# Performance work log

Hardware: AMD Instinct MI355X
Metric: run time of the kernel (lower is better)

## Reference

```python
import jax, jax.numpy as jnp
import numpy as np
from jax import lax

SAMPLE_RATE = 0.25
RADIUS = 0.5
NSAMPLE = 32
MLP = [64 + 3, 64, 128]  # use_xyz adds 3 to first width


def setup_inputs() -> dict:
    key = jax.random.key(0)
    ks = jax.random.split(key, 8)
    B, N, C = 8, 8192, 64
    pos = jax.random.normal(ks[0], (B, N, 3), dtype=jnp.float32)
    features = jax.random.normal(ks[1], (B, C, N), dtype=jnp.float32)
    # shared MLP (1x1 Conv2d with bias, ReLU), He-scaled init
    w0 = jax.random.normal(ks[2], (MLP[1], MLP[0]), jnp.float32) * (2.0 / MLP[0]) ** 0.5
    b0 = jnp.zeros((MLP[1],), jnp.float32)
    w1 = jax.random.normal(ks[3], (MLP[1], MLP[1]), jnp.float32) * (2.0 / MLP[1]) ** 0.5
    b1 = jnp.zeros((MLP[1],), jnp.float32)
    w2 = jax.random.normal(ks[4], (MLP[2], MLP[1]), jnp.float32) * (2.0 / MLP[1]) ** 0.5
    b2 = jnp.zeros((MLP[2],), jnp.float32)
    return {"pos": pos, "features": features, "w0": w0, "b0": b0,
            "w1": w1, "b1": b1, "w2": w2, "b2": b2}


def furthest_point_sample(pos, npoint):
    """pos: (B,N,3) -> idx (B,npoint) int32, greedy FPS starting at index 0."""
    B, N, _ = pos.shape
    init_idx = jnp.zeros((B,), jnp.int32)
    init_d = jnp.full((B, N), 1e10, jnp.float32)

    def step(carry, _):
        dists, last = carry
        p_last = jnp.take_along_axis(pos, last[:, None, None], axis=1)  # (B,1,3)
        d = jnp.sum((pos - p_last) ** 2, axis=-1)                        # (B,N)
        dists = jnp.minimum(dists, d)
        nxt = jnp.argmax(dists, axis=-1).astype(jnp.int32)
        return (dists, nxt), nxt

    (_, _), rest = lax.scan(step, (init_d, init_idx), None, length=npoint - 1)
    return jnp.concatenate([init_idx[None, :], rest], axis=0).T  # (B,npoint)


def ball_query(pos, new_xyz, nsample, radius):
    """pos (B,N,3), new_xyz (B,S,3) -> idx (B,S,nsample): first nsample pts
    within radius, padded with the first hit (0 if no hit), as in PointNet2 CUDA."""
    B, N, _ = pos.shape
    d2 = jnp.sum((new_xyz[:, :, None, :] - pos[:, None, :, :]) ** 2, axis=-1)  # (B,S,N)
    cand = jnp.where(d2 < radius * radius,
                     jnp.arange(N, dtype=jnp.int32)[None, None, :], N)
    neg_top, _ = lax.top_k(-cand, nsample)     # smallest nsample indices
    idx = -neg_top                              # ascending index order
    first = idx[..., :1]
    pad = jnp.where(first == N, 0, first)
    return jnp.where(idx == N, pad, idx)


def reference(pos, features, w0, b0, w1, b1, w2, b2):
    B, N, _ = pos.shape
    npoint = int(N * SAMPLE_RATE)
    fps_idx = furthest_point_sample(pos, npoint)                         # (B,S)
    new_xyz = jax.vmap(lambda p, i: p[i])(pos, fps_idx)                  # (B,S,3)

    idx = ball_query(pos, new_xyz, NSAMPLE, RADIUS)                      # (B,S,K)
    grouped_xyz = jax.vmap(lambda p, i: p[i])(pos, idx)                  # (B,S,K,3)
    rel_xyz = grouped_xyz - new_xyz[:, :, None, :]                       # (B,S,K,3)
    grouped_feat = jax.vmap(lambda f, i: f[:, i])(features, idx)         # (B,C,S,K)
    x = jnp.concatenate([rel_xyz.transpose(0, 3, 1, 2), grouped_feat], axis=1)  # (B,3+C,S,K)

    def conv_relu(x, w, b):  # 1x1 conv + bias + ReLU
        y = jnp.einsum('oc,bcsk->bosk', w, x) + b[None, :, None, None]
        return jax.nn.relu(y)

    x = conv_relu(x, w0, b0)
    x = conv_relu(x, w1, b1)
    x = conv_relu(x, w2, b2)
    new_features = jnp.max(x, axis=-1)                                   # (B,mlp[-1],S)
    return new_xyz, new_features
```

## Files before the change

kernel.cpp:

```cpp
#include <hip/hip_runtime.h>

#define NB 8
#define NPTS 8192
#define NC_FEAT 64
#define NS 2048
#define NK 32

typedef float v2f __attribute__((ext_vector_type(2)));

__device__ __forceinline__ float d2_ref(float px, float py, float pz,
                                        float qx, float qy, float qz) {
  float dx = __fsub_rn(px, qx);
  float dy = __fsub_rn(py, qy);
  float dz = __fsub_rn(pz, qz);
  return __fadd_rn(__fadd_rn(__fmul_rn(dx, dx), __fmul_rn(dy, dy)),
                   __fmul_rn(dz, dz));
}

#define DPP_KEYMAX(key, ctrl)                                                 \
  {                                                                           \
    unsigned _lo = (unsigned)__builtin_amdgcn_update_dpp(                     \
        0, (int)(unsigned)(key), (ctrl), 0xf, 0xf, true);                     \
    unsigned _hi = (unsigned)__builtin_amdgcn_update_dpp(                     \
        0, (int)(unsigned)((key) >> 32), (ctrl), 0xf, 0xf, true);             \
    unsigned long long _o = ((unsigned long long)_hi << 32) | _lo;            \
    if (_o > (key)) (key) = _o;                                               \
  }

__global__ __launch_bounds__(512)
void k_fps(const float* __restrict__ pos, float* __restrict__ new_xyz) {
#pragma clang fp contract(off)
  __shared__ __align__(16) float smem[3 * NPTS + 64];
  const int tid = threadIdx.x;
  const int b = blockIdx.x;
  float* sx = smem;
  float* sy = smem + NPTS;
  float* sz = smem + 2 * NPTS;
  unsigned long long* rk = (unsigned long long*)(smem + 3 * NPTS);

  const float* p = pos + (size_t)b * NPTS * 3;
  for (int i = tid; i < NPTS; i += 512) {
    sx[i] = p[3 * i + 0];
    sy[i] = p[3 * i + 1];
    sz[i] = p[3 * i + 2];
  }
  if (tid < 32) rk[tid] = 0ull;
  __syncthreads();

  const int base = tid * 16;
  v2f px[8], py[8], pz[8], di[8];
#pragma unroll
  for (int k = 0; k < 8; ++k) {
    px[k] = (v2f){sx[base + 2 * k], sx[base + 2 * k + 1]};
    py[k] = (v2f){sy[base + 2 * k], sy[base + 2 * k + 1]};
    pz[k] = (v2f){sz[base + 2 * k], sz[base + 2 * k + 1]};
    di[k] = (v2f){1e10f, 1e10f};
  }
  if (tid == 0) {
    new_xyz[((size_t)b * NS) * 3 + 0] = sx[0];
    new_xyz[((size_t)b * NS) * 3 + 1] = sy[0];
    new_xyz[((size_t)b * NS) * 3 + 2] = sz[0];
  }

  const int lane = tid & 63;
  const int wave = tid >> 6;
  const unsigned nbase = ~(unsigned)base;
  int last = 0, buf = 0;

  for (int it = 1; it < NS; ++it) {
    float qx = sx[last], qy = sy[last], qz = sz[last];
#pragma unroll
    for (int k = 0; k < 8; ++k) {
      v2f dx = px[k] - qx;
      v2f dy = py[k] - qy;
      v2f dz = pz[k] - qz;
      v2f d2 = (dx * dx + dy * dy) + dz * dz;
      di[k] = __builtin_elementwise_min(di[k], d2);
    }
    v2f m0 = __builtin_elementwise_max(di[0], di[1]);
    v2f m1 = __builtin_elementwise_max(di[2], di[3]);
    v2f m2 = __builtin_elementwise_max(di[4], di[5]);
    v2f m3 = __builtin_elementwise_max(di[6], di[7]);
    v2f m4 = __builtin_elementwise_max(m0, m1);
    v2f m5 = __builtin_elementwise_max(m2, m3);
    v2f m6 = __builtin_elementwise_max(m4, m5);
    float bd = fmaxf(m6.x, m6.y);
    int bj = 0;
#pragma unroll
    for (int j = 15; j >= 0; --j) {
      float v = (j & 1) ? di[j >> 1].y : di[j >> 1].x;
      if (v == bd) bj = j;
    }
    unsigned long long key =
        ((unsigned long long)__float_as_uint(bd) << 32) |
        (unsigned)(nbase - (unsigned)bj);
    DPP_KEYMAX(key, 0x111);
    DPP_KEYMAX(key, 0x112);
    DPP_KEYMAX(key, 0x114);
    DPP_KEYMAX(key, 0x118);
    DPP_KEYMAX(key, 0x142);
    DPP_KEYMAX(key, 0x143);
    if (lane == 63) rk[buf * 16 + wave] = key;
    __syncthreads();
    key = rk[buf * 16 + (lane & 15)];
    DPP_KEYMAX(key, 0x111);
    DPP_KEYMAX(key, 0x112);
    DPP_KEYMAX(key, 0x114);
    DPP_KEYMAX(key, 0x118);
    int fi = (int)~(unsigned)__builtin_amdgcn_readlane((int)(unsigned)key, 15);
    last = fi;
    buf ^= 1;
    if (tid == 0) {
      new_xyz[((size_t)b * NS + it) * 3 + 0] = sx[fi];
      new_xyz[((size_t)b * NS + it) * 3 + 1] = sy[fi];
      new_xyz[((size_t)b * NS + it) * 3 + 2] = sz[fi];
    }
  }
}

__global__ __launch_bounds__(256)
void k_tp(const float* __restrict__ feat, const float* __restrict__ w0,
          const float* __restrict__ w1, const float* __restrict__ w2,
          float* __restrict__ featT, float* __restrict__ wT) {
  __shared__ float tile[64 * 65];
  const int tid = threadIdx.x;
  if (blockIdx.x < NB * (NPTS / 64)) {
    const int t = blockIdx.x;
    const int b = t >> 7;
    const int n0 = (t & 127) << 6;
    const int col = tid & 63;
    const int r0 = tid >> 6;
#pragma unroll
    for (int q = 0; q < 16; ++q) {
      int c = r0 + q * 4;
      tile[c * 65 + col] = feat[((size_t)b * NC_FEAT + c) * NPTS + n0 + col];
    }
    __syncthreads();
#pragma unroll
    for (int q = 0; q < 16; ++q) {
      int r = r0 + q * 4;
      featT[((size_t)b * NPTS + n0 + r) * 64 + col] = tile[col * 65 + r];
    }
  } else {
    for (int i = tid; i < 67 * 64; i += 256)
      wT[i] = w0[(i & 63) * 67 + (i >> 6)];
    for (int i = tid; i < 64 * 64; i += 256)
      wT[67 * 64 + i] = w1[(i & 63) * 64 + (i >> 6)];
    for (int i = tid; i < 64 * 128; i += 256)
      wT[67 * 64 + 64 * 64 + i] = w2[(i & 127) * 64 + (i >> 7)];
  }
}

__global__ __launch_bounds__(256)
void k_ball(const float* __restrict__ pos, const float* __restrict__ nxyz,
            int* __restrict__ ballidx) {
  const int wid = (blockIdx.x * 256 + threadIdx.x) >> 6;
  const int lane = threadIdx.x & 63;
  const int b = wid >> 11;
  const float qx = nxyz[wid * 3 + 0];
  const float qy = nxyz[wid * 3 + 1];
  const float qz = nxyz[wid * 3 + 2];
  const float* p = pos + (size_t)b * NPTS * 3;
  int* outp = ballidx + (size_t)wid * NK;

  int cnt = 0;
  int firstidx = 0x7fffffff;
  for (int n0 = 0; n0 < NPTS; n0 += 64) {
    const int i = n0 + lane;
    float d2 = d2_ref(p[3 * i], p[3 * i + 1], p[3 * i + 2], qx, qy, qz);
    bool hit = d2 < 0.25f;
    unsigned long long mask = __ballot(hit);
    int pre = __popcll(mask & ((1ull << lane) - 1ull));
    int slot = cnt + pre;
    if (hit && slot < NK) outp[slot] = i;
    if (hit && slot == 0) firstidx = i;
    cnt += __popcll(mask);
    if (cnt >= NK) break;
  }
#pragma unroll
  for (int m = 32; m >= 1; m >>= 1)
    firstidx = min(firstidx, __shfl_xor(firstidx, m, 64));
  int pad = (firstidx == 0x7fffffff) ? 0 : firstidx;
  int start = cnt < NK ? cnt : NK;
  if (lane < NK && lane >= start) outp[lane] = pad;
}

#define MLP_FMA16(wr, xc, acc)                                   \
  _Pragma("unroll") for (int o4 = 0; o4 < 16; ++o4) {            \
    float4 w = (wr)[o4];                                         \
    (acc)[o4 * 4 + 0] = fmaf(w.x, (xc), (acc)[o4 * 4 + 0]);      \
    (acc)[o4 * 4 + 1] = fmaf(w.y, (xc), (acc)[o4 * 4 + 1]);      \
    (acc)[o4 * 4 + 2] = fmaf(w.z, (xc), (acc)[o4 * 4 + 2]);      \
    (acc)[o4 * 4 + 3] = fmaf(w.w, (xc), (acc)[o4 * 4 + 3]);      \
  }

__global__ __launch_bounds__(256)
void k_mlp(const float* __restrict__ pos, const float* __restrict__ featT,
           const float* __restrict__ wT, const float* __restrict__ b0,
           const float* __restrict__ b1, const float* __restrict__ b2,
           const int* __restrict__ ballidx, const float* __restrict__ nxyz,
           float* __restrict__ outf) {
  __shared__ float xs[64 * 256];
  const int tid = threadIdx.x;
  const int g = blockIdx.x * 256 + tid;
  const int s = (g >> 5) & (NS - 1);
  const int b = g >> 16;

  const int idx = ballidx[g];
  const float qx = nxyz[((size_t)b * NS + s) * 3 + 0];
  const float qy = nxyz[((size_t)b * NS + s) * 3 + 1];
  const float qz = nxyz[((size_t)b * NS + s) * 3 + 2];
  const float* pp = pos + ((size_t)b * NPTS + idx) * 3;
  const float x0 = __fsub_rn(pp[0], qx);
  const float x1 = __fsub_rn(pp[1], qy);
  const float x2 = __fsub_rn(pp[2], qz);

  const float4* fT = (const float4*)(featT + ((size_t)b * NPTS + idx) * 64);
#pragma unroll
  for (int c4 = 0; c4 < 16; ++c4) {
    float4 v = fT[c4];
    xs[(c4 * 4 + 0) * 256 + tid] = v.x;
    xs[(c4 * 4 + 1) * 256 + tid] = v.y;
    xs[(c4 * 4 + 2) * 256 + tid] = v.z;
    xs[(c4 * 4 + 3) * 256 + tid] = v.w;
  }

  const float* wt0 = wT;
  const float* wt1 = wT + 67 * 64;
  const float* wt2 = wT + 67 * 64 + 64 * 64;

  float acc[64];
#pragma unroll
  for (int o = 0; o < 64; ++o) acc[o] = b0[o];
  {
    const float xr0 = x0, xr1 = x1, xr2 = x2;
    const float4* wr;
    wr = (const float4*)(wt0 + 0 * 64); MLP_FMA16(wr, xr0, acc);
    wr = (const float4*)(wt0 + 1 * 64); MLP_FMA16(wr, xr1, acc);
    wr = (const float4*)(wt0 + 2 * 64); MLP_FMA16(wr, xr2, acc);
  }
  for (int c = 0; c < 64; ++c) {
    float xc = xs[c * 256 + tid];
    const float4* wr = (const float4*)(wt0 + (3 + c) * 64);
    MLP_FMA16(wr, xc, acc);
  }
#pragma unroll
  for (int o = 0; o < 64; ++o) xs[o * 256 + tid] = fmaxf(acc[o], 0.0f);

#pragma unroll
  for (int o = 0; o < 64; ++o) acc[o] = b1[o];
  for (int c = 0; c < 64; ++c) {
    float xc = xs[c * 256 + tid];
    const float4* wr = (const float4*)(wt1 + c * 64);
    MLP_FMA16(wr, xc, acc);
  }
#pragma unroll
  for (int o = 0; o < 64; ++o) xs[o * 256 + tid] = fmaxf(acc[o], 0.0f);

#pragma unroll
  for (int h = 0; h < 2; ++h) {
#pragma unroll
    for (int o = 0; o < 64; ++o) acc[o] = b2[h * 64 + o];
    for (int c = 0; c < 64; ++c) {
      float xc = xs[c * 256 + tid];
      const float4* wr = (const float4*)(wt2 + c * 128 + h * 64);
      MLP_FMA16(wr, xc, acc);
    }
#pragma unroll
    for (int o = 0; o < 64; ++o) {
      float v = fmaxf(acc[o], 0.0f);
      v = fmaxf(v, __shfl_xor(v, 16, 64));
      v = fmaxf(v, __shfl_xor(v, 8, 64));
      v = fmaxf(v, __shfl_xor(v, 4, 64));
      v = fmaxf(v, __shfl_xor(v, 2, 64));
      v = fmaxf(v, __shfl_xor(v, 1, 64));
      if ((tid & 31) == 0)
        outf[((size_t)b * 128 + h * 64 + o) * NS + s] = v;
    }
  }
}

extern "C" void kernel_launch(void* const* d_in, const int* in_sizes, int n_in,
                              void* d_out, int out_size, void* d_ws,
                              size_t ws_size, hipStream_t stream) {
  const float* pos = (const float*)d_in[0];
  const float* feat = (const float*)d_in[1];
  const float* w0 = (const float*)d_in[2];
  const float* b0 = (const float*)d_in[3];
  const float* w1 = (const float*)d_in[4];
  const float* b1 = (const float*)d_in[5];
  const float* w2 = (const float*)d_in[6];
  const float* b2 = (const float*)d_in[7];

  float* out = (float*)d_out;
  float* new_xyz = out;
  float* new_feat = out + (size_t)NB * NS * 3;

  int* ballidx = (int*)d_ws;
  float* featT = (float*)d_ws + (size_t)NB * NS * NK;
  float* wT = featT + (size_t)NB * NPTS * 64;

  hipLaunchKernelGGL(k_tp, dim3(NB * (NPTS / 64) + 1), dim3(256), 0, stream,
                     feat, w0, w1, w2, featT, wT);
  hipLaunchKernelGGL(k_fps, dim3(NB), dim3(512), 0, stream, pos, new_xyz);
  hipLaunchKernelGGL(k_ball, dim3((NB * NS) / 4), dim3(256), 0, stream, pos,
                     new_xyz, ballidx);
  hipLaunchKernelGGL(k_mlp, dim3((NB * NS * NK) / 256), dim3(256), 0, stream,
                     pos, featT, wT, b0, b1, b2, ballidx, new_xyz, new_feat);
}
```

Measured before the change: 2.457 ms.

## Morton-sort points in FPS and skip distance updates for far thread clusters

The FPS kernel now computes a bounding box, quantizes points to 10-bit Morton codes and bitonic-sorts them in shared memory so each thread owns a spatially compact cluster. Each thread keeps a bounding sphere and skips its distance-update and local argmax when the newly selected point is too far away to lower any of its distances, reusing its cached key. Tie-breaking keys now encode the original index so results match the reference's lowest-index argmax. This adds a one-off sort with many barriers and more shared memory, and the skip check depends on the float margins being conservative.

```diff
diff --git a/kernel.cpp b/kernel.cpp
--- a/kernel.cpp
+++ b/kernel.cpp
@@ -27,93 +27,224 @@
     if (_o > (key)) (key) = _o;                                               \
   }
 
+#define DPP_FMIN(v, ctrl)                                                     \
+  {                                                                           \
+    float _o = __int_as_float(__builtin_amdgcn_update_dpp(                    \
+        __float_as_int(v), __float_as_int(v), (ctrl), 0xf, 0xf, false));      \
+    (v) = fminf((v), _o);                                                     \
+  }
+#define DPP_FMAX(v, ctrl)                                                     \
+  {                                                                           \
+    float _o = __int_as_float(__builtin_amdgcn_update_dpp(                    \
+        __float_as_int(v), __float_as_int(v), (ctrl), 0xf, 0xf, false));      \
+    (v) = fmaxf((v), _o);                                                     \
+  }
+#define DPP_RED6_FMIN(v) \
+  DPP_FMIN(v, 0x111); DPP_FMIN(v, 0x112); DPP_FMIN(v, 0x114); \
+  DPP_FMIN(v, 0x118); DPP_FMIN(v, 0x142); DPP_FMIN(v, 0x143)
+#define DPP_RED6_FMAX(v) \
+  DPP_FMAX(v, 0x111); DPP_FMAX(v, 0x112); DPP_FMAX(v, 0x114); \
+  DPP_FMAX(v, 0x118); DPP_FMAX(v, 0x142); DPP_FMAX(v, 0x143)
+
+__device__ __forceinline__ unsigned msp(unsigned x) {
+  x &= 0x3FF;
+  x = (x | (x << 16)) & 0x030000FF;
+  x = (x | (x << 8)) & 0x0300F00F;
+  x = (x | (x << 4)) & 0x030C30C3;
+  x = (x | (x << 2)) & 0x09249249;
+  return x;
+}
+
 __global__ __launch_bounds__(512)
 void k_fps(const float* __restrict__ pos, float* __restrict__ new_xyz) {
 #pragma clang fp contract(off)
-  __shared__ __align__(16) float smem[3 * NPTS + 64];
-  const int tid = threadIdx.x;
-  const int b = blockIdx.x;
+  __shared__ __align__(16) float smem[4 * NPTS + 128];
   float* sx = smem;
   float* sy = smem + NPTS;
   float* sz = smem + 2 * NPTS;
-  unsigned long long* rk = (unsigned long long*)(smem + 3 * NPTS);
-
+  unsigned* K = (unsigned*)smem;
+  unsigned* P = (unsigned*)(smem + 3 * NPTS);
+  unsigned long long* rk = (unsigned long long*)(smem + 4 * NPTS);
+  float* wavebb = smem + 4 * NPTS + 64;
+  float* bbx = smem + 4 * NPTS + 64 + 48;
+  int* last0p = (int*)(smem + 4 * NPTS + 64 + 48 + 6);
+
+  const int tid = threadIdx.x;
+  const int b = blockIdx.x;
+  const int lane = tid & 63;
+  const int wave = tid >> 6;
   const float* p = pos + (size_t)b * NPTS * 3;
+
+  float mnx = 3e38f, mny = 3e38f, mnz = 3e38f;
+  float mxx = -3e38f, mxy = -3e38f, mxz = -3e38f;
   for (int i = tid; i < NPTS; i += 512) {
-    sx[i] = p[3 * i + 0];
-    sy[i] = p[3 * i + 1];
-    sz[i] = p[3 * i + 2];
+    float x = p[3 * i], y = p[3 * i + 1], z = p[3 * i + 2];
+    mnx = fminf(mnx, x); mxx = fmaxf(mxx, x);
+    mny = fminf(mny, y); mxy = fmaxf(mxy, y);
+    mnz = fminf(mnz, z); mxz = fmaxf(mxz, z);
+  }
+  DPP_RED6_FMIN(mnx); DPP_RED6_FMIN(mny); DPP_RED6_FMIN(mnz);
+  DPP_RED6_FMAX(mxx); DPP_RED6_FMAX(mxy); DPP_RED6_FMAX(mxz);
+  if (lane == 63) {
+    wavebb[wave * 6 + 0] = mnx; wavebb[wave * 6 + 1] = mny;
+    wavebb[wave * 6 + 2] = mnz; wavebb[wave * 6 + 3] = mxx;
+    wavebb[wave * 6 + 4] = mxy; wavebb[wave * 6 + 5] = mxz;
+  }
+  __syncthreads();
+  if (tid == 0) {
+    float a0 = 3e38f, a1 = 3e38f, a2 = 3e38f;
+    float a3 = -3e38f, a4 = -3e38f, a5 = -3e38f;
+    for (int w = 0; w < 8; ++w) {
+      a0 = fminf(a0, wavebb[w * 6 + 0]); a1 = fminf(a1, wavebb[w * 6 + 1]);
+      a2 = fminf(a2, wavebb[w * 6 + 2]); a3 = fmaxf(a3, wavebb[w * 6 + 3]);
+      a4 = fmaxf(a4, wavebb[w * 6 + 4]); a5 = fmaxf(a5, wavebb[w * 6 + 5]);
+    }
+    bbx[0] = a0; bbx[1] = a1; bbx[2] = a2;
+    bbx[3] = 1023.0f / fmaxf(a3 - a0, 1e-30f);
+    bbx[4] = 1023.0f / fmaxf(a4 - a1, 1e-30f);
+    bbx[5] = 1023.0f / fmaxf(a5 - a2, 1e-30f);
+  }
+  __syncthreads();
+  const float ox = bbx[0], oy = bbx[1], oz = bbx[2];
+  const float gx = bbx[3], gy = bbx[4], gz = bbx[5];
+
+  for (int i = tid; i < NPTS; i += 512) {
+    float x = p[3 * i], y = p[3 * i + 1], z = p[3 * i + 2];
+    unsigned ux = (unsigned)fminf(fmaxf((x - ox) * gx, 0.0f), 1023.0f);
+    unsigned uy = (unsigned)fminf(fmaxf((y - oy) * gy, 0.0f), 1023.0f);
+    unsigned uz = (unsigned)fminf(fmaxf((z - oz) * gz, 0.0f), 1023.0f);
+    K[i] = msp(ux) | (msp(uy) << 1) | (msp(uz) << 2);
+    P[i] = (unsigned)i;
+  }
+
+  for (int k2 = 2; k2 <= NPTS; k2 <<= 1) {
+    for (int j = k2 >> 1; j > 0; j >>= 1) {
+      __syncthreads();
+      for (int t = 0; t < 16; ++t) {
+        int i = t * 512 + tid;
+        int ixj = i ^ j;
+        if (ixj > i) {
+          unsigned a = K[i], c = K[ixj];
+          bool up = ((i & k2) == 0);
+          if ((a > c) == up) {
+            K[i] = c; K[ixj] = a;
+            unsigned pa = P[i]; P[i] = P[ixj]; P[ixj] = pa;
+          }
+        }
+      }
+    }
+  }
+  __syncthreads();
+
+  for (int i = tid; i < NPTS; i += 512) {
+    unsigned u = P[i];
+    if (u == 0) *last0p = i;
+    sx[i] = p[3 * u];
+    sy[i] = p[3 * u + 1];
+    sz[i] = p[3 * u + 2];
   }
   if (tid < 32) rk[tid] = 0ull;
   __syncthreads();
 
   const int base = tid * 16;
   v2f px[8], py[8], pz[8], di[8];
+  unsigned opk[8];
 #pragma unroll
   for (int k = 0; k < 8; ++k) {
     px[k] = (v2f){sx[base + 2 * k], sx[base + 2 * k + 1]};
     py[k] = (v2f){sy[base + 2 * k], sy[base + 2 * k + 1]};
     pz[k] = (v2f){sz[base + 2 * k], sz[base + 2 * k + 1]};
     di[k] = (v2f){1e10f, 1e10f};
-  }
+    opk[k] = (P[base + 2 * k] & 0xFFFF) | (P[base + 2 * k + 1] << 16);
+  }
+  float lmnx = 3e38f, lmny = 3e38f, lmnz = 3e38f;
+  float lmxx = -3e38f, lmxy = -3e38f, lmxz = -3e38f;
+#pragma unroll
+  for (int k = 0; k < 8; ++k) {
+    lmnx = fminf(lmnx, fminf(px[k].x, px[k].y));
+    lmxx = fmaxf(lmxx, fmaxf(px[k].x, px[k].y));
+    lmny = fminf(lmny, fminf(py[k].x, py[k].y));
+    lmxy = fmaxf(lmxy, fmaxf(py[k].x, py[k].y));
+    lmnz = fminf(lmnz, fminf(pz[k].x, pz[k].y));
+    lmxz = fmaxf(lmxz, fmaxf(pz[k].x, pz[k].y));
+  }
+  const float cx = (lmnx + lmxx) * 0.5f;
+  const float cy = (lmny + lmxy) * 0.5f;
+  const float cz = (lmnz + lmxz) * 0.5f;
+  float r2m = 0.0f;
+#pragma unroll
+  for (int k = 0; k < 8; ++k) {
+    r2m = fmaxf(r2m, d2_ref(px[k].x, py[k].x, pz[k].x, cx, cy, cz));
+    r2m = fmaxf(r2m, d2_ref(px[k].y, py[k].y, pz[k].y, cx, cy, cz));
+  }
+  const float r = sqrtf(r2m) * 1.001f;
+  float T = 3.4e38f;
+  unsigned long long key = 0;
+
+  int last = *last0p;
   if (tid == 0) {
-    new_xyz[((size_t)b * NS) * 3 + 0] = sx[0];
-    new_xyz[((size_t)b * NS) * 3 + 1] = sy[0];
-    new_xyz[((size_t)b * NS) * 3 + 2] = sz[0];
-  }
-
-  const int lane = tid & 63;
-  const int wave = tid >> 6;
-  const unsigned nbase = ~(unsigned)base;
-  int last = 0, buf = 0;
+    new_xyz[((size_t)b * NS) * 3 + 0] = sx[last];
+    new_xyz[((size_t)b * NS) * 3 + 1] = sy[last];
+    new_xyz[((size_t)b * NS) * 3 + 2] = sz[last];
+  }
+  int buf = 0;
 
   for (int it = 1; it < NS; ++it) {
     float qx = sx[last], qy = sy[last], qz = sz[last];
-#pragma unroll
-    for (int k = 0; k < 8; ++k) {
-      v2f dx = px[k] - qx;
-      v2f dy = py[k] - qy;
-      v2f dz = pz[k] - qz;
-      v2f d2 = (dx * dx + dy * dy) + dz * dz;
-      di[k] = __builtin_elementwise_min(di[k], d2);
-    }
-    v2f m0 = __builtin_elementwise_max(di[0], di[1]);
-    v2f m1 = __builtin_elementwise_max(di[2], di[3]);
-    v2f m2 = __builtin_elementwise_max(di[4], di[5]);
-    v2f m3 = __builtin_elementwise_max(di[6], di[7]);
-    v2f m4 = __builtin_elementwise_max(m0, m1);
-    v2f m5 = __builtin_elementwise_max(m2, m3);
-    v2f m6 = __builtin_elementwise_max(m4, m5);
-    float bd = fmaxf(m6.x, m6.y);
-    int bj = 0;
-#pragma unroll
-    for (int j = 15; j >= 0; --j) {
-      float v = (j & 1) ? di[j >> 1].y : di[j >> 1].x;
-      if (v == bd) bj = j;
-    }
-    unsigned long long key =
-        ((unsigned long long)__float_as_uint(bd) << 32) |
-        (unsigned)(nbase - (unsigned)bj);
-    DPP_KEYMAX(key, 0x111);
-    DPP_KEYMAX(key, 0x112);
-    DPP_KEYMAX(key, 0x114);
-    DPP_KEYMAX(key, 0x118);
-    DPP_KEYMAX(key, 0x142);
-    DPP_KEYMAX(key, 0x143);
-    if (lane == 63) rk[buf * 16 + wave] = key;
+    float ddx = cx - qx, ddy = cy - qy, ddz = cz - qz;
+    float dc2 = ddx * ddx + ddy * ddy + ddz * ddz;
+    if (dc2 <= T) {
+#pragma unroll
+      for (int k = 0; k < 8; ++k) {
+        v2f dx = px[k] - qx;
+        v2f dy = py[k] - qy;
+        v2f dz = pz[k] - qz;
+        v2f d2 = (dx * dx + dy * dy) + dz * dz;
+        di[k] = __builtin_elementwise_min(di[k], d2);
+      }
+      v2f m0 = __builtin_elementwise_max(di[0], di[1]);
+      v2f m1 = __builtin_elementwise_max(di[2], di[3]);
+      v2f m2 = __builtin_elementwise_max(di[4], di[5]);
+      v2f m3 = __builtin_elementwise_max(di[6], di[7]);
+      v2f m4 = __builtin_elementwise_max(m0, m1);
+      v2f m5 = __builtin_elementwise_max(m2, m3);
+      v2f m6 = __builtin_elementwise_max(m4, m5);
+      float bd = fmaxf(m6.x, m6.y);
+      int bj = 0;
+      unsigned oj = 0;
+#pragma unroll
+      for (int j = 15; j >= 0; --j) {
+        float v = (j & 1) ? di[j >> 1].y : di[j >> 1].x;
+        unsigned o = (j & 1) ? (opk[j >> 1] >> 16) : (opk[j >> 1] & 0xFFFF);
+        if (v == bd) { bj = j; oj = o; }
+      }
+      key = ((unsigned long long)__float_as_uint(bd) << 32) |
+            ((unsigned long long)((~oj) & 0x1FFFu) << 13) |
+            (unsigned)(base + bj);
+      float t1 = sqrtf(bd) * 1.001f + r;
+      T = t1 * t1 * 1.002f;
+    }
+    unsigned long long wk = key;
+    DPP_KEYMAX(wk, 0x111);
+    DPP_KEYMAX(wk, 0x112);
+    DPP_KEYMAX(wk, 0x114);
+    DPP_KEYMAX(wk, 0x118);
+    DPP_KEYMAX(wk, 0x142);
+    DPP_KEYMAX(wk, 0x143);
+    if (lane == 63) rk[buf * 16 + wave] = wk;
     __syncthreads();
-    key = rk[buf * 16 + (lane & 15)];
-    DPP_KEYMAX(key, 0x111);
-    DPP_KEYMAX(key, 0x112);
-    DPP_KEYMAX(key, 0x114);
-    DPP_KEYMAX(key, 0x118);
-    int fi = (int)~(unsigned)__builtin_amdgcn_readlane((int)(unsigned)key, 15);
-    last = fi;
+    wk = rk[buf * 16 + (lane & 15)];
+    DPP_KEYMAX(wk, 0x111);
+    DPP_KEYMAX(wk, 0x112);
+    DPP_KEYMAX(wk, 0x114);
+    DPP_KEYMAX(wk, 0x118);
+    last = (int)((unsigned)__builtin_amdgcn_readlane((int)(unsigned)wk, 15) &
+                 0x1FFFu);
     buf ^= 1;
     if (tid == 0) {
-      new_xyz[((size_t)b * NS + it) * 3 + 0] = sx[fi];
-      new_xyz[((size_t)b * NS + it) * 3 + 1] = sy[fi];
-      new_xyz[((size_t)b * NS + it) * 3 + 2] = sz[fi];
+      new_xyz[((size_t)b * NS + it) * 3 + 0] = sx[last];
+      new_xyz[((size_t)b * NS + it) * 3 + 1] = sy[last];
+      new_xyz[((size_t)b * NS + it) * 3 + 2] = sz[last];
     }
   }
 }
```

Result: slower. 3.304 ms (+34.5%).

## Shrink FPS block to 256 threads with 32 points per thread and inline-asm distance

Applied to the files above, without the earlier changes.

The furthest-point-sampling kernel now runs 4 waves of 256 threads, each holding 32 points in registers instead of 16. Fewer waves shorten the cross-wave reduction: only 4 partial keys go through shared memory, and the second DPP stage drops to two steps. The distance update is written as packed-f32 inline assembly, and a running argmax is kept inside the loop instead of a separate max tree plus equality scan. The trade is double the serial per-thread work on each iteration in exchange for cheaper synchronisation; the FPS launch is only 8 blocks, so latency is set by the per-block critical path.

```diff
diff --git a/kernel.cpp b/kernel.cpp
--- a/kernel.cpp
+++ b/kernel.cpp
@@ -27,33 +27,34 @@
     if (_o > (key)) (key) = _o;                                               \
   }
 
-__global__ __launch_bounds__(512)
+__global__ __launch_bounds__(256)
 void k_fps(const float* __restrict__ pos, float* __restrict__ new_xyz) {
 #pragma clang fp contract(off)
-  __shared__ __align__(16) float smem[3 * NPTS + 64];
-  const int tid = threadIdx.x;
-  const int b = blockIdx.x;
+  __shared__ __align__(16) float smem[3 * NPTS + 16];
   float* sx = smem;
   float* sy = smem + NPTS;
   float* sz = smem + 2 * NPTS;
   unsigned long long* rk = (unsigned long long*)(smem + 3 * NPTS);
 
+  const int tid = threadIdx.x;
+  const int b = blockIdx.x;
   const float* p = pos + (size_t)b * NPTS * 3;
-  for (int i = tid; i < NPTS; i += 512) {
+
+  for (int i = tid; i < NPTS; i += 256) {
     sx[i] = p[3 * i + 0];
     sy[i] = p[3 * i + 1];
     sz[i] = p[3 * i + 2];
   }
-  if (tid < 32) rk[tid] = 0ull;
+  if (tid < 8) rk[tid] = 0ull;
   __syncthreads();
 
-  const int base = tid * 16;
-  v2f px[8], py[8], pz[8], di[8];
-#pragma unroll
-  for (int k = 0; k < 8; ++k) {
-    px[k] = (v2f){sx[base + 2 * k], sx[base + 2 * k + 1]};
-    py[k] = (v2f){sy[base + 2 * k], sy[base + 2 * k + 1]};
-    pz[k] = (v2f){sz[base + 2 * k], sz[base + 2 * k + 1]};
+  const int base = tid * 32;
+  v2f px[16], py[16], pz[16], di[16];
+#pragma unroll
+  for (int k = 0; k < 16; ++k) {
+    px[k] = *(const v2f*)&sx[base + 2 * k];
+    py[k] = *(const v2f*)&sy[base + 2 * k];
+    pz[k] = *(const v2f*)&sz[base + 2 * k];
     di[k] = (v2f){1e10f, 1e10f};
   }
   if (tid == 0) {
@@ -64,50 +65,47 @@
 
   const int lane = tid & 63;
   const int wave = tid >> 6;
-  const unsigned nbase = ~(unsigned)base;
   int last = 0, buf = 0;
 
   for (int it = 1; it < NS; ++it) {
     float qx = sx[last], qy = sy[last], qz = sz[last];
-#pragma unroll
-    for (int k = 0; k < 8; ++k) {
-      v2f dx = px[k] - qx;
-      v2f dy = py[k] - qy;
-      v2f dz = pz[k] - qz;
-      v2f d2 = (dx * dx + dy * dy) + dz * dz;
-      di[k] = __builtin_elementwise_min(di[k], d2);
-    }
-    v2f m0 = __builtin_elementwise_max(di[0], di[1]);
-    v2f m1 = __builtin_elementwise_max(di[2], di[3]);
-    v2f m2 = __builtin_elementwise_max(di[4], di[5]);
-    v2f m3 = __builtin_elementwise_max(di[6], di[7]);
-    v2f m4 = __builtin_elementwise_max(m0, m1);
-    v2f m5 = __builtin_elementwise_max(m2, m3);
-    v2f m6 = __builtin_elementwise_max(m4, m5);
-    float bd = fmaxf(m6.x, m6.y);
+    v2f nqx = (v2f){-qx, -qx};
+    v2f nqy = (v2f){-qy, -qy};
+    v2f nqz = (v2f){-qz, -qz};
+    float bd = -1.0f;
     int bj = 0;
 #pragma unroll
-    for (int j = 15; j >= 0; --j) {
-      float v = (j & 1) ? di[j >> 1].y : di[j >> 1].x;
-      if (v == bd) bj = j;
+    for (int k = 0; k < 16; ++k) {
+      v2f t0, t1, t2, d2v;
+      asm("v_pk_add_f32 %0, %4, %7\n\t"
+          "v_pk_add_f32 %1, %5, %8\n\t"
+          "v_pk_add_f32 %2, %6, %9\n\t"
+          "v_pk_mul_f32 %0, %0, %0\n\t"
+          "v_pk_mul_f32 %1, %1, %1\n\t"
+          "v_pk_mul_f32 %2, %2, %2\n\t"
+          "v_pk_add_f32 %3, %0, %1\n\t"
+          "v_pk_add_f32 %3, %3, %2"
+          : "=&v"(t0), "=&v"(t1), "=&v"(t2), "=&v"(d2v)
+          : "v"(px[k]), "v"(py[k]), "v"(pz[k]), "v"(nqx), "v"(nqy), "v"(nqz));
+      di[k] = __builtin_elementwise_min(di[k], d2v);
+      if (di[k].x > bd) { bd = di[k].x; bj = 2 * k; }
+      if (di[k].y > bd) { bd = di[k].y; bj = 2 * k + 1; }
     }
     unsigned long long key =
         ((unsigned long long)__float_as_uint(bd) << 32) |
-        (unsigned)(nbase - (unsigned)bj);
+        (unsigned)~(unsigned)(base + bj);
     DPP_KEYMAX(key, 0x111);
     DPP_KEYMAX(key, 0x112);
     DPP_KEYMAX(key, 0x114);
     DPP_KEYMAX(key, 0x118);
     DPP_KEYMAX(key, 0x142);
     DPP_KEYMAX(key, 0x143);
-    if (lane == 63) rk[buf * 16 + wave] = key;
+    if (lane == 63) rk[buf * 4 + wave] = key;
     __syncthreads();
-    key = rk[buf * 16 + (lane & 15)];
+    key = rk[buf * 4 + (lane & 3)];
     DPP_KEYMAX(key, 0x111);
     DPP_KEYMAX(key, 0x112);
-    DPP_KEYMAX(key, 0x114);
-    DPP_KEYMAX(key, 0x118);
-    int fi = (int)~(unsigned)__builtin_amdgcn_readlane((int)(unsigned)key, 15);
+    int fi = (int)~(unsigned)__builtin_amdgcn_readlane((int)(unsigned)key, 3);
     last = fi;
     buf ^= 1;
     if (tid == 0) {
@@ -302,7 +300,7 @@
 
   hipLaunchKernelGGL(k_tp, dim3(NB * (NPTS / 64) + 1), dim3(256), 0, stream,
                      feat, w0, w1, w2, featT, wT);
-  hipLaunchKernelGGL(k_fps, dim3(NB), dim3(512), 0, stream, pos, new_xyz);
+  hipLaunchKernelGGL(k_fps, dim3(NB), dim3(256), 0, stream, pos, new_xyz);
   hipLaunchKernelGGL(k_ball, dim3((NB * NS) / 4), dim3(256), 0, stream, pos,
                      new_xyz, ballidx);
   hipLaunchKernelGGL(k_mlp, dim3((NB * NS * NK) / 256), dim3(256), 0, stream,
```

Result: slower. 2.524 ms (+2.7%).

## Fuse FPS, ball query and MLP into one persistent kernel with progress flags

Applied to the files above, without the earlier changes.

Replaces the separate FPS, ball-query and MLP launches with one persistent kernel. The first 8 blocks run FPS and publish sampled centroids plus a progress counter through global atomics. The remaining blocks pull 16-centroid tasks from an atomic queue, spin until FPS has reached those centroids, then run ball query into shared memory and the MLP. This overlaps the serial FPS phase with downstream work and removes the ball-index round trip through global memory, but it depends on co-residency of the FPS blocks with the spinning workers and adds polling overhead.

```diff
diff --git a/kernel.cpp b/kernel.cpp
--- a/kernel.cpp
+++ b/kernel.cpp
@@ -5,8 +5,16 @@
 #define NC_FEAT 64
 #define NS 2048
 #define NK 32
+#define NTASK (NB * NS)
 
 typedef float v2f __attribute__((ext_vector_type(2)));
+
+#define WS_QUEUE 0
+#define WS_PROG 64
+#define WS_XY64 4096
+#define WS_Z32 (4096 + 131072)
+#define WS_FEATT (4096 + 131072 + 65536)
+#define WS_WT (WS_FEATT + (size_t)NB * NPTS * 64 * 4)
 
 __device__ __forceinline__ float d2_ref(float px, float py, float pz,
                                         float qx, float qy, float qz) {
@@ -27,102 +35,22 @@
     if (_o > (key)) (key) = _o;                                               \
   }
 
-__global__ __launch_bounds__(512)
-void k_fps(const float* __restrict__ pos, float* __restrict__ new_xyz) {
-#pragma clang fp contract(off)
-  __shared__ __align__(16) float smem[3 * NPTS + 64];
-  const int tid = threadIdx.x;
-  const int b = blockIdx.x;
-  float* sx = smem;
-  float* sy = smem + NPTS;
-  float* sz = smem + 2 * NPTS;
-  unsigned long long* rk = (unsigned long long*)(smem + 3 * NPTS);
-
-  const float* p = pos + (size_t)b * NPTS * 3;
-  for (int i = tid; i < NPTS; i += 512) {
-    sx[i] = p[3 * i + 0];
-    sy[i] = p[3 * i + 1];
-    sz[i] = p[3 * i + 2];
-  }
-  if (tid < 32) rk[tid] = 0ull;
-  __syncthreads();
-
-  const int base = tid * 16;
-  v2f px[8], py[8], pz[8], di[8];
-#pragma unroll
-  for (int k = 0; k < 8; ++k) {
-    px[k] = (v2f){sx[base + 2 * k], sx[base + 2 * k + 1]};
-    py[k] = (v2f){sy[base + 2 * k], sy[base + 2 * k + 1]};
-    pz[k] = (v2f){sz[base + 2 * k], sz[base + 2 * k + 1]};
-    di[k] = (v2f){1e10f, 1e10f};
-  }
-  if (tid == 0) {
-    new_xyz[((size_t)b * NS) * 3 + 0] = sx[0];
-    new_xyz[((size_t)b * NS) * 3 + 1] = sy[0];
-    new_xyz[((size_t)b * NS) * 3 + 2] = sz[0];
-  }
-
-  const int lane = tid & 63;
-  const int wave = tid >> 6;
-  const unsigned nbase = ~(unsigned)base;
-  int last = 0, buf = 0;
-
-  for (int it = 1; it < NS; ++it) {
-    float qx = sx[last], qy = sy[last], qz = sz[last];
-#pragma unroll
-    for (int k = 0; k < 8; ++k) {
-      v2f dx = px[k] - qx;
-      v2f dy = py[k] - qy;
-      v2f dz = pz[k] - qz;
-      v2f d2 = (dx * dx + dy * dy) + dz * dz;
-      di[k] = __builtin_elementwise_min(di[k], d2);
-    }
-    v2f m0 = __builtin_elementwise_max(di[0], di[1]);
-    v2f m1 = __builtin_elementwise_max(di[2], di[3]);
-    v2f m2 = __builtin_elementwise_max(di[4], di[5]);
-    v2f m3 = __builtin_elementwise_max(di[6], di[7]);
-    v2f m4 = __builtin_elementwise_max(m0, m1);
-    v2f m5 = __builtin_elementwise_max(m2, m3);
-    v2f m6 = __builtin_elementwise_max(m4, m5);
-    float bd = fmaxf(m6.x, m6.y);
-    int bj = 0;
-#pragma unroll
-    for (int j = 15; j >= 0; --j) {
-      float v = (j & 1) ? di[j >> 1].y : di[j >> 1].x;
-      if (v == bd) bj = j;
-    }
-    unsigned long long key =
-        ((unsigned long long)__float_as_uint(bd) << 32) |
-        (unsigned)(nbase - (unsigned)bj);
-    DPP_KEYMAX(key, 0x111);
-    DPP_KEYMAX(key, 0x112);
-    DPP_KEYMAX(key, 0x114);
-    DPP_KEYMAX(key, 0x118);
-    DPP_KEYMAX(key, 0x142);
-    DPP_KEYMAX(key, 0x143);
-    if (lane == 63) rk[buf * 16 + wave] = key;
-    __syncthreads();
-    key = rk[buf * 16 + (lane & 15)];
-    DPP_KEYMAX(key, 0x111);
-    DPP_KEYMAX(key, 0x112);
-    DPP_KEYMAX(key, 0x114);
-    DPP_KEYMAX(key, 0x118);
-    int fi = (int)~(unsigned)__builtin_amdgcn_readlane((int)(unsigned)key, 15);
-    last = fi;
-    buf ^= 1;
-    if (tid == 0) {
-      new_xyz[((size_t)b * NS + it) * 3 + 0] = sx[fi];
-      new_xyz[((size_t)b * NS + it) * 3 + 1] = sy[fi];
-      new_xyz[((size_t)b * NS + it) * 3 + 2] = sz[fi];
-    }
-  }
-}
+#define MLP_FMA16(wr, xc, acc)                                   \
+  _Pragma("unroll") for (int o4 = 0; o4 < 16; ++o4) {            \
+    float4 w = (wr)[o4];                                         \
+    (acc)[o4 * 4 + 0] = fmaf(w.x, (xc), (acc)[o4 * 4 + 0]);      \
+    (acc)[o4 * 4 + 1] = fmaf(w.y, (xc), (acc)[o4 * 4 + 1]);      \
+    (acc)[o4 * 4 + 2] = fmaf(w.z, (xc), (acc)[o4 * 4 + 2]);      \
+    (acc)[o4 * 4 + 3] = fmaf(w.w, (xc), (acc)[o4 * 4 + 3]);      \
+  }
 
 __global__ __launch_bounds__(256)
 void k_tp(const float* __restrict__ feat, const float* __restrict__ w0,
           const float* __restrict__ w1, const float* __restrict__ w2,
-          float* __restrict__ featT, float* __restrict__ wT) {
+          char* __restrict__ ws) {
   __shared__ float tile[64 * 65];
+  float* featT = (float*)(ws + WS_FEATT);
+  float* wT = (float*)(ws + WS_WT);
   const int tid = threadIdx.x;
   if (blockIdx.x < NB * (NPTS / 64)) {
     const int t = blockIdx.x;
@@ -142,6 +70,7 @@
       featT[((size_t)b * NPTS + n0 + r) * 64 + col] = tile[col * 65 + r];
     }
   } else {
+    if (tid < 24) ((int*)ws)[tid] = 0;
     for (int i = tid; i < 67 * 64; i += 256)
       wT[i] = w0[(i & 63) * 67 + (i >> 6)];
     for (int i = tid; i < 64 * 64; i += 256)
@@ -151,132 +80,268 @@
   }
 }
 
-__global__ __launch_bounds__(256)
-void k_ball(const float* __restrict__ pos, const float* __restrict__ nxyz,
-            int* __restrict__ ballidx) {
-  const int wid = (blockIdx.x * 256 + threadIdx.x) >> 6;
-  const int lane = threadIdx.x & 63;
-  const int b = wid >> 11;
-  const float qx = nxyz[wid * 3 + 0];
-  const float qy = nxyz[wid * 3 + 1];
-  const float qz = nxyz[wid * 3 + 2];
-  const float* p = pos + (size_t)b * NPTS * 3;
-  int* outp = ballidx + (size_t)wid * NK;
-
-  int cnt = 0;
-  int firstidx = 0x7fffffff;
-  for (int n0 = 0; n0 < NPTS; n0 += 64) {
-    const int i = n0 + lane;
-    float d2 = d2_ref(p[3 * i], p[3 * i + 1], p[3 * i + 2], qx, qy, qz);
-    bool hit = d2 < 0.25f;
-    unsigned long long mask = __ballot(hit);
-    int pre = __popcll(mask & ((1ull << lane) - 1ull));
-    int slot = cnt + pre;
-    if (hit && slot < NK) outp[slot] = i;
-    if (hit && slot == 0) firstidx = i;
-    cnt += __popcll(mask);
-    if (cnt >= NK) break;
-  }
-#pragma unroll
-  for (int m = 32; m >= 1; m >>= 1)
-    firstidx = min(firstidx, __shfl_xor(firstidx, m, 64));
-  int pad = (firstidx == 0x7fffffff) ? 0 : firstidx;
-  int start = cnt < NK ? cnt : NK;
-  if (lane < NK && lane >= start) outp[lane] = pad;
-}
-
-#define MLP_FMA16(wr, xc, acc)                                   \
-  _Pragma("unroll") for (int o4 = 0; o4 < 16; ++o4) {            \
-    float4 w = (wr)[o4];                                         \
-    (acc)[o4 * 4 + 0] = fmaf(w.x, (xc), (acc)[o4 * 4 + 0]);      \
-    (acc)[o4 * 4 + 1] = fmaf(w.y, (xc), (acc)[o4 * 4 + 1]);      \
-    (acc)[o4 * 4 + 2] = fmaf(w.z, (xc), (acc)[o4 * 4 + 2]);      \
-    (acc)[o4 * 4 + 3] = fmaf(w.w, (xc), (acc)[o4 * 4 + 3]);      \
-  }
-
-__global__ __launch_bounds__(256)
-void k_mlp(const float* __restrict__ pos, const float* __restrict__ featT,
-           const float* __restrict__ wT, const float* __restrict__ b0,
-           const float* __restrict__ b1, const float* __restrict__ b2,
-           const int* __restrict__ ballidx, const float* __restrict__ nxyz,
-           float* __restrict__ outf) {
-  __shared__ float xs[64 * 256];
-  const int tid = threadIdx.x;
-  const int g = blockIdx.x * 256 + tid;
-  const int s = (g >> 5) & (NS - 1);
-  const int b = g >> 16;
-
-  const int idx = ballidx[g];
-  const float qx = nxyz[((size_t)b * NS + s) * 3 + 0];
-  const float qy = nxyz[((size_t)b * NS + s) * 3 + 1];
-  const float qz = nxyz[((size_t)b * NS + s) * 3 + 2];
-  const float* pp = pos + ((size_t)b * NPTS + idx) * 3;
-  const float x0 = __fsub_rn(pp[0], qx);
-  const float x1 = __fsub_rn(pp[1], qy);
-  const float x2 = __fsub_rn(pp[2], qz);
-
-  const float4* fT = (const float4*)(featT + ((size_t)b * NPTS + idx) * 64);
-#pragma unroll
-  for (int c4 = 0; c4 < 16; ++c4) {
-    float4 v = fT[c4];
-    xs[(c4 * 4 + 0) * 256 + tid] = v.x;
-    xs[(c4 * 4 + 1) * 256 + tid] = v.y;
-    xs[(c4 * 4 + 2) * 256 + tid] = v.z;
-    xs[(c4 * 4 + 3) * 256 + tid] = v.w;
-  }
-
-  const float* wt0 = wT;
-  const float* wt1 = wT + 67 * 64;
-  const float* wt2 = wT + 67 * 64 + 64 * 64;
-
-  float acc[64];
-#pragma unroll
-  for (int o = 0; o < 64; ++o) acc[o] = b0[o];
-  {
-    const float xr0 = x0, xr1 = x1, xr2 = x2;
-    const float4* wr;
-    wr = (const float4*)(wt0 + 0 * 64); MLP_FMA16(wr, xr0, acc);
-    wr = (const float4*)(wt0 + 1 * 64); MLP_FMA16(wr, xr1, acc);
-    wr = (const float4*)(wt0 + 2 * 64); MLP_FMA16(wr, xr2, acc);
-  }
-  for (int c = 0; c < 64; ++c) {
-    float xc = xs[c * 256 + tid];
-    const float4* wr = (const float4*)(wt0 + (3 + c) * 64);
-    MLP_FMA16(wr, xc, acc);
-  }
-#pragma unroll
-  for (int o = 0; o < 64; ++o) xs[o * 256 + tid] = fmaxf(acc[o], 0.0f);
-
-#pragma unroll
-  for (int o = 0; o < 64; ++o) acc[o] = b1[o];
-  for (int c = 0; c < 64; ++c) {
-    float xc = xs[c * 256 + tid];
-    const float4* wr = (const float4*)(wt1 + c * 64);
-    MLP_FMA16(wr, xc, acc);
-  }
-#pragma unroll
-  for (int o = 0; o < 64; ++o) xs[o * 256 + tid] = fmaxf(acc[o], 0.0f);
-
-#pragma unroll
-  for (int h = 0; h < 2; ++h) {
-#pragma unroll
-    for (int o = 0; o < 64; ++o) acc[o] = b2[h * 64 + o];
-    for (int c = 0; c < 64; ++c) {
-      float xc = xs[c * 256 + tid];
-      const float4* wr = (const float4*)(wt2 + c * 128 + h * 64);
-      MLP_FMA16(wr, xc, acc);
-    }
-#pragma unroll
-    for (int o = 0; o < 64; ++o) {
-      float v = fmaxf(acc[o], 0.0f);
-      v = fmaxf(v, __shfl_xor(v, 16, 64));
-      v = fmaxf(v, __shfl_xor(v, 8, 64));
-      v = fmaxf(v, __shfl_xor(v, 4, 64));
-      v = fmaxf(v, __shfl_xor(v, 2, 64));
-      v = fmaxf(v, __shfl_xor(v, 1, 64));
-      if ((tid & 31) == 0)
-        outf[((size_t)b * 128 + h * 64 + o) * NS + s] = v;
-    }
+__global__ __launch_bounds__(512)
+void k_fused(const float* __restrict__ pos, const float* __restrict__ b0,
+             const float* __restrict__ b1, const float* __restrict__ b2,
+             char* __restrict__ ws, float* __restrict__ new_xyz,
+             float* __restrict__ outf) {
+#pragma clang fp contract(off)
+  __shared__ __align__(16) float smf[33360];
+  int* queue = (int*)ws;
+  int* progress = (int*)(ws + WS_PROG);
+  unsigned long long* xy64 = (unsigned long long*)(ws + WS_XY64);
+  unsigned* z32 = (unsigned*)(ws + WS_Z32);
+  const float* featT = (const float*)(ws + WS_FEATT);
+  const float* wT = (const float*)(ws + WS_WT);
+  const int wtid = threadIdx.x;
+
+  if (blockIdx.x < NB) {
+    float* sx = smf;
+    float* sy = smf + NPTS;
+    float* sz = smf + 2 * NPTS;
+    unsigned long long* rk = (unsigned long long*)(smf + 3 * NPTS);
+    const int tid = wtid;
+    const int b = blockIdx.x;
+    const float* p = pos + (size_t)b * NPTS * 3;
+
+    for (int i = tid; i < NPTS; i += 512) {
+      sx[i] = p[3 * i + 0];
+      sy[i] = p[3 * i + 1];
+      sz[i] = p[3 * i + 2];
+    }
+    if (tid < 32) rk[tid] = 0ull;
+    __syncthreads();
+
+    const int base = tid * 16;
+    v2f px[8], py[8], pz[8], di[8];
+#pragma unroll
+    for (int k = 0; k < 8; ++k) {
+      px[k] = *(const v2f*)&sx[base + 2 * k];
+      py[k] = *(const v2f*)&sy[base + 2 * k];
+      pz[k] = *(const v2f*)&sz[base + 2 * k];
+      di[k] = (v2f){1e10f, 1e10f};
+    }
+    if (tid == 0) {
+      new_xyz[((size_t)b * NS) * 3 + 0] = sx[0];
+      new_xyz[((size_t)b * NS) * 3 + 1] = sy[0];
+      new_xyz[((size_t)b * NS) * 3 + 2] = sz[0];
+      unsigned long long xy = ((unsigned long long)__float_as_uint(sy[0]) << 32) |
+                              __float_as_uint(sx[0]);
+      __hip_atomic_store(&xy64[b * NS + 0], xy, __ATOMIC_RELAXED,
+                         __HIP_MEMORY_SCOPE_AGENT);
+      __hip_atomic_store(&z32[b * NS + 0], __float_as_uint(sz[0]),
+                         __ATOMIC_RELAXED, __HIP_MEMORY_SCOPE_AGENT);
+    }
+
+    const int lane = tid & 63;
+    const int wave = tid >> 6;
+    int last = 0, buf = 0;
+
+    for (int it = 1; it < NS; ++it) {
+      float qx = sx[last], qy = sy[last], qz = sz[last];
+#pragma unroll
+      for (int k = 0; k < 8; ++k) {
+        v2f dx = px[k] - qx;
+        v2f dy = py[k] - qy;
+        v2f dz = pz[k] - qz;
+        v2f d2 = (dx * dx + dy * dy) + dz * dz;
+        di[k] = __builtin_elementwise_min(di[k], d2);
+      }
+      v2f m0 = __builtin_elementwise_max(di[0], di[1]);
+      v2f m1 = __builtin_elementwise_max(di[2], di[3]);
+      v2f m2 = __builtin_elementwise_max(di[4], di[5]);
+      v2f m3 = __builtin_elementwise_max(di[6], di[7]);
+      v2f m4 = __builtin_elementwise_max(m0, m1);
+      v2f m5 = __builtin_elementwise_max(m2, m3);
+      v2f m6 = __builtin_elementwise_max(m4, m5);
+      float bd = fmaxf(m6.x, m6.y);
+      int bj = 0;
+#pragma unroll
+      for (int j = 15; j >= 0; --j) {
+        float v = (j & 1) ? di[j >> 1].y : di[j >> 1].x;
+        if (v == bd) bj = j;
+      }
+      unsigned long long key =
+          ((unsigned long long)__float_as_uint(bd) << 32) |
+          (unsigned)~(unsigned)(base + bj);
+      DPP_KEYMAX(key, 0x111);
+      DPP_KEYMAX(key, 0x112);
+      DPP_KEYMAX(key, 0x114);
+      DPP_KEYMAX(key, 0x118);
+      DPP_KEYMAX(key, 0x142);
+      DPP_KEYMAX(key, 0x143);
+      if (lane == 63) rk[buf * 16 + wave] = key;
+      __syncthreads();
+      key = rk[buf * 16 + (lane & 15)];
+      DPP_KEYMAX(key, 0x111);
+      DPP_KEYMAX(key, 0x112);
+      DPP_KEYMAX(key, 0x114);
+      DPP_KEYMAX(key, 0x118);
+      int fi = (int)~(unsigned)__builtin_amdgcn_readlane((int)(unsigned)key, 15);
+      last = fi;
+      buf ^= 1;
+      if (tid == 0) {
+        float fx = sx[fi], fy = sy[fi], fz = sz[fi];
+        new_xyz[((size_t)b * NS + it) * 3 + 0] = fx;
+        new_xyz[((size_t)b * NS + it) * 3 + 1] = fy;
+        new_xyz[((size_t)b * NS + it) * 3 + 2] = fz;
+        unsigned long long xy =
+            ((unsigned long long)__float_as_uint(fy) << 32) | __float_as_uint(fx);
+        __hip_atomic_store(&xy64[b * NS + it], xy, __ATOMIC_RELAXED,
+                           __HIP_MEMORY_SCOPE_AGENT);
+        __hip_atomic_store(&z32[b * NS + it], __float_as_uint(fz),
+                           __ATOMIC_RELAXED, __HIP_MEMORY_SCOPE_AGENT);
+        if ((it & 31) == 31)
+          __hip_atomic_store(&progress[b], it + 1, __ATOMIC_RELEASE,
+                             __HIP_MEMORY_SCOPE_AGENT);
+      }
+    }
+    return;
+  }
+
+  float* xs0 = smf;
+  int* sidx = (int*)(smf + 32768);
+  float* snx = smf + 32768 + 512;
+  int* sbase = (int*)(smf + 32768 + 512 + 64);
+  const int lane = wtid & 63;
+  const int w = wtid >> 6;
+
+  for (;;) {
+    if (wtid == 0) *sbase = atomicAdd(queue, 16);
+    __syncthreads();
+    const int base_t = *sbase;
+    if (base_t >= NTASK) break;
+    const int sEnd = ((base_t + 15) >> 3) + 1;
+    if (wtid < 64) {
+      int pr;
+      do {
+        __builtin_amdgcn_s_sleep(2);
+        pr = (lane < 8) ? __hip_atomic_load(&progress[lane], __ATOMIC_ACQUIRE,
+                                            __HIP_MEMORY_SCOPE_AGENT)
+                        : 0x7fffffff;
+      } while (!__all(pr >= sEnd));
+    }
+    __syncthreads();
+    if (wtid < 16) {
+      int t = base_t + wtid, bb = t & 7, ss = t >> 3;
+      unsigned long long xy = __hip_atomic_load(
+          &xy64[bb * NS + ss], __ATOMIC_RELAXED, __HIP_MEMORY_SCOPE_AGENT);
+      unsigned z = __hip_atomic_load(&z32[bb * NS + ss], __ATOMIC_RELAXED,
+                                     __HIP_MEMORY_SCOPE_AGENT);
+      snx[wtid * 4 + 0] = __uint_as_float((unsigned)xy);
+      snx[wtid * 4 + 1] = __uint_as_float((unsigned)(xy >> 32));
+      snx[wtid * 4 + 2] = __uint_as_float(z);
+    }
+    __syncthreads();
+#pragma unroll
+    for (int tt = 0; tt < 2; ++tt) {
+      const int tl = w * 2 + tt;
+      const int bb = (base_t + tl) & 7;
+      const float qx = snx[tl * 4 + 0];
+      const float qy = snx[tl * 4 + 1];
+      const float qz = snx[tl * 4 + 2];
+      const float* p = pos + (size_t)bb * NPTS * 3;
+      int cnt = 0;
+      int firstidx = 0x7fffffff;
+      for (int n0 = 0; n0 < NPTS; n0 += 64) {
+        const int i = n0 + lane;
+        float d2 = d2_ref(p[3 * i], p[3 * i + 1], p[3 * i + 2], qx, qy, qz);
+        bool hit = d2 < 0.25f;
+        unsigned long long mask = __ballot(hit);
+        int pre = __popcll(mask & ((1ull << lane) - 1ull));
+        int slot = cnt + pre;
+        if (hit && slot < NK) sidx[tl * 32 + slot] = i;
+        if (hit && slot == 0) firstidx = i;
+        cnt += __popcll(mask);
+        if (cnt >= NK) break;
+      }
+#pragma unroll
+      for (int m = 32; m >= 1; m >>= 1)
+        firstidx = min(firstidx, __shfl_xor(firstidx, m, 64));
+      int pad = (firstidx == 0x7fffffff) ? 0 : firstidx;
+      int start = cnt < NK ? cnt : NK;
+      if (lane < NK && lane >= start) sidx[tl * 32 + lane] = pad;
+    }
+    __syncthreads();
+    {
+      const int grp = wtid >> 8;
+      const int tidl = wtid & 255;
+      const int tl = grp * 8 + (tidl >> 5);
+      const int t = base_t + tl;
+      const int bb = t & 7;
+      const int ss = t >> 3;
+      const int k = tidl & 31;
+      float* xs = xs0 + grp * 16384;
+
+      const int idx = sidx[tl * 32 + k];
+      const float qx = snx[tl * 4 + 0];
+      const float qy = snx[tl * 4 + 1];
+      const float qz = snx[tl * 4 + 2];
+      const float* pp = pos + ((size_t)bb * NPTS + idx) * 3;
+      const float x0 = __fsub_rn(pp[0], qx);
+      const float x1 = __fsub_rn(pp[1], qy);
+      const float x2 = __fsub_rn(pp[2], qz);
+
+      const float4* fT = (const float4*)(featT + ((size_t)bb * NPTS + idx) * 64);
+#pragma unroll
+      for (int c4 = 0; c4 < 16; ++c4) {
+        float4 v = fT[c4];
+        xs[(c4 * 4 + 0) * 256 + tidl] = v.x;
+        xs[(c4 * 4 + 1) * 256 + tidl] = v.y;
+        xs[(c4 * 4 + 2) * 256 + tidl] = v.z;
+        xs[(c4 * 4 + 3) * 256 + tidl] = v.w;
+      }
+      const float* wt0 = wT;
+      const float* wt1 = wT + 67 * 64;
+      const float* wt2 = wT + 67 * 64 + 64 * 64;
+      float acc[64];
+#pragma unroll
+      for (int o = 0; o < 64; ++o) acc[o] = b0[o];
+      {
+        const float4* wr;
+        wr = (const float4*)(wt0 + 0 * 64); MLP_FMA16(wr, x0, acc);
+        wr = (const float4*)(wt0 + 1 * 64); MLP_FMA16(wr, x1, acc);
+        wr = (const float4*)(wt0 + 2 * 64); MLP_FMA16(wr, x2, acc);
+      }
+      for (int c = 0; c < 64; ++c) {
+        float xc = xs[c * 256 + tidl];
+        const float4* wr = (const float4*)(wt0 + (3 + c) * 64);
+        MLP_FMA16(wr, xc, acc);
+      }
+#pragma unroll
+      for (int o = 0; o < 64; ++o) xs[o * 256 + tidl] = fmaxf(acc[o], 0.0f);
+#pragma unroll
+      for (int o = 0; o < 64; ++o) acc[o] = b1[o];
+      for (int c = 0; c < 64; ++c) {
+        float xc = xs[c * 256 + tidl];
+        const float4* wr = (const float4*)(wt1 + c * 64);
+        MLP_FMA16(wr, xc, acc);
+      }
+#pragma unroll
+      for (int o = 0; o < 64; ++o) xs[o * 256 + tidl] = fmaxf(acc[o], 0.0f);
+#pragma unroll
+      for (int h = 0; h < 2; ++h) {
+#pragma unroll
+        for (int o = 0; o < 64; ++o) acc[o] = b2[h * 64 + o];
+        for (int c = 0; c < 64; ++c) {
+          float xc = xs[c * 256 + tidl];
+          const float4* wr = (const float4*)(wt2 + c * 128 + h * 64);
+          MLP_FMA16(wr, xc, acc);
+        }
+#pragma unroll
+        for (int o = 0; o < 64; ++o) {
+          float v = fmaxf(acc[o], 0.0f);
+          v = fmaxf(v, __shfl_xor(v, 16, 64));
+          v = fmaxf(v, __shfl_xor(v, 8, 64));
+          v = fmaxf(v, __shfl_xor(v, 4, 64));
+          v = fmaxf(v, __shfl_xor(v, 2, 64));
+          v = fmaxf(v, __shfl_xor(v, 1, 64));
+          if ((tidl & 31) == 0)
+            outf[((size_t)bb * 128 + h * 64 + o) * NS + ss] = v;
+        }
+      }
+    }
+    __syncthreads();
   }
 }
 
@@ -295,16 +360,10 @@
   float* out = (float*)d_out;
   float* new_xyz = out;
   float* new_feat = out + (size_t)NB * NS * 3;
-
-  int* ballidx = (int*)d_ws;
-  float* featT = (float*)d_ws + (size_t)NB * NS * NK;
-  float* wT = featT + (size_t)NB * NPTS * 64;
+  char* ws = (char*)d_ws;
 
   hipLaunchKernelGGL(k_tp, dim3(NB * (NPTS / 64) + 1), dim3(256), 0, stream,
-                     feat, w0, w1, w2, featT, wT);
-  hipLaunchKernelGGL(k_fps, dim3(NB), dim3(512), 0, stream, pos, new_xyz);
-  hipLaunchKernelGGL(k_ball, dim3((NB * NS) / 4), dim3(256), 0, stream, pos,
-                     new_xyz, ballidx);
-  hipLaunchKernelGGL(k_mlp, dim3((NB * NS * NK) / 256), dim3(256), 0, stream,
-                     pos, featT, wT, b0, b1, b2, ballidx, new_xyz, new_feat);
+                     feat, w0, w1, w2, ws);
+  hipLaunchKernelGGL(k_fused, dim3(256), dim3(512), 0, stream, pos, b0, b1,
+                     b2, ws, new_xyz, new_feat);
 }
```

Result: faster. 2.342 ms (-4.7%).
